# Kernel optimization log

Measured on AMD Instinct MI355X. Metric: run time of the kernel, lower is better.

Reference implementation:

```python
import jax, jax.numpy as jnp
import numpy as np

B, N, D, L, K, H = 64, 576, 768, 64, 5, 8  # batch, tokens, dim, out_token_len, knn k, heads
HD = D // H
SCALE = HD ** -0.5


def layer_norm(x, g, b, eps=1e-5):
    m = jnp.mean(x, axis=-1, keepdims=True)
    v = jnp.mean((x - m) ** 2, axis=-1, keepdims=True)
    return (x - m) * jax.lax.rsqrt(v + eps) * g + b


def cluster(feat, noise):
    # DPC-KNN: pairwise distances, k-NN density, parent distance, peak selection
    sq = jnp.sum(feat * feat, axis=-1)  # [B,N]
    dm = sq[:, :, None] + sq[:, None, :] - 2.0 * jnp.einsum('bnd,bmd->bnm', feat, feat)
    dm = jnp.sqrt(jnp.maximum(dm, 0.0)) / jnp.sqrt(jnp.asarray(D, feat.dtype))  # [B,N,N]
    neg_near, _ = jax.lax.top_k(-dm, K)                       # k smallest distances (negated)
    density = jnp.exp(-jnp.mean(neg_near ** 2, axis=-1))      # [B,N]
    density = density + noise * 1e-6                          # deterministic tie-break
    mask = (density[:, None, :] > density[:, :, None]).astype(feat.dtype)
    dist_max = jnp.max(dm.reshape(dm.shape[0], -1), axis=-1)[:, None, None]
    dist = jnp.min(dm * mask + dist_max * (1.0 - mask), axis=-1)  # [B,N]
    score = dist * density
    _, idx_down = jax.lax.top_k(score, L)                     # [B,L] cluster centers
    dm_down = jnp.take_along_axis(dm, idx_down[:, :, None], axis=1)  # [B,L,N]
    idx_cluster = jnp.argmin(dm_down, axis=1)                 # [B,N] assign to nearest center
    idx_cluster = idx_cluster.at[jnp.arange(dm.shape[0])[:, None], idx_down].set(
        jnp.arange(L)[None, :])
    return idx_cluster


def merger(feat, idx_cluster, token_score):
    b, n, d = feat.shape
    idx = (idx_cluster + jnp.arange(b)[:, None] * L).reshape(-1)       # [B*N]
    tw = jnp.exp(token_score)                                          # [B,N,1]
    all_w = jax.ops.segment_sum(tw.reshape(-1, 1), idx, num_segments=b * L) + 1e-6
    norm_w = tw / all_w[idx].reshape(b, n, 1)
    merged = jax.ops.segment_sum((feat * norm_w).reshape(-1, d), idx, num_segments=b * L)
    return merged.reshape(b, L, d)


def setup_inputs() -> dict:
    key = jax.random.key(0)
    ks = jax.random.split(key, 16)
    s = 0.02
    return {
        'x': jax.random.normal(ks[0], (B, N, D), jnp.float32),
        'density_noise': jax.random.uniform(ks[1], (B, N), jnp.float32),
        'norm1_g': jnp.ones((D,), jnp.float32),
        'norm1_b': jnp.zeros((D,), jnp.float32),
        'score_w': s * jax.random.normal(ks[2], (D, 1), jnp.float32),
        'score_b': jnp.zeros((1,), jnp.float32),
        'wq': s * jax.random.normal(ks[3], (D, D), jnp.float32),
        'wk': s * jax.random.normal(ks[4], (D, D), jnp.float32),
        'wv': s * jax.random.normal(ks[5], (D, D), jnp.float32),
        'proj_w': s * jax.random.normal(ks[6], (D, D), jnp.float32),
        'proj_b': jnp.zeros((D,), jnp.float32),
        'norm2_g': jnp.ones((D,), jnp.float32),
        'norm2_b': jnp.zeros((D,), jnp.float32),
        'fc1_w': s * jax.random.normal(ks[7], (D, 4 * D), jnp.float32),
        'fc1_b': jnp.zeros((4 * D,), jnp.float32),
        'fc2_w': s * jax.random.normal(ks[8], (4 * D, D), jnp.float32),
        'fc2_b': jnp.zeros((D,), jnp.float32),
    }


def reference(x, density_noise, norm1_g, norm1_b, score_w, score_b, wq, wk, wv,
              proj_w, proj_b, norm2_g, norm2_b, fc1_w, fc1_b, fc2_w, fc2_b):
    xn = layer_norm(x, norm1_g, norm1_b)                 # [B,N,D]
    token_score = xn @ score_w + score_b                 # [B,N,1]
    idx_cluster = cluster(jax.lax.stop_gradient(xn), density_noise)  # no-grad in torch
    q_input = merger(xn, idx_cluster, token_score)       # [B,L,D]
    kv = xn
    # STMAttention: cross-attn with token_score bias added to logits
    q = (q_input @ wq).reshape(B, L, H, HD).transpose(0, 2, 1, 3)
    k = (kv @ wk).reshape(B, N, H, HD).transpose(0, 2, 1, 3)
    v = (kv @ wv).reshape(B, N, H, HD).transpose(0, 2, 1, 3)
    dots = jnp.einsum('bhid,bhjd->bhij', q, k) * SCALE   # [B,H,L,N]
    bias = token_score[:, :, 0][:, None, None, :]        # [B,1,1,N]
    attn = jax.nn.softmax(dots + bias, axis=-1)
    out = jnp.einsum('bhij,bhjd->bhid', attn, v)
    out = out.transpose(0, 2, 1, 3).reshape(B, L, D)
    out = out @ proj_w + proj_b
    feature = q_input + out
    h = layer_norm(feature, norm2_g, norm2_b)
    h = jax.nn.gelu(h @ fc1_w + fc1_b, approximate=False) @ fc2_w + fc2_b
    return feature + h
```

## Files before the change

kernel.cpp:

```cpp
#include <hip/hip_runtime.h>
#include <math.h>

#define B_   64
#define N_   576
#define D_   768
#define L_   64
#define H_   8
#define HD_  96
#define NB_  (B_*N_)
#define ML_  (B_*L_)
#define KV_STRIDE_ 1536
#define SCALE_ 0.10206207f
#define INV_SQRT_D_ 0.03608439182f
#define LO_SCALE_ 4.8828125e-4f

typedef __attribute__((ext_vector_type(8))) _Float16 half8v;
typedef __attribute__((ext_vector_type(4))) float floatx4;

__device__ __forceinline__ unsigned short f2h(float f) {
  _Float16 h = (_Float16)f;
  unsigned short u; __builtin_memcpy(&u, &h, 2);
  return u;
}
__device__ __forceinline__ float h2f(unsigned short u) {
  _Float16 h; __builtin_memcpy(&h, &u, 2);
  return (float)h;
}
__device__ __forceinline__ void gload_lds16(const void* g, void* l) {
  __builtin_amdgcn_global_load_lds(
      (const __attribute__((address_space(1))) unsigned*)g,
      (__attribute__((address_space(3))) unsigned*)l, 16, 0, 0);
}

__global__ __launch_bounds__(256) void k_ln1(const float* __restrict__ x,
    const float* __restrict__ g, const float* __restrict__ bt,
    const float* __restrict__ sw, const float* __restrict__ sb,
    unsigned short* __restrict__ xh, unsigned short* __restrict__ xl,
    float* __restrict__ ts, float* __restrict__ sq)
{
  int row = blockIdx.x, tid = threadIdx.x;
  const float* xr = x + (size_t)row * D_;
  float v0 = xr[tid], v1 = xr[tid + 256], v2 = xr[tid + 512];
  __shared__ float r1[256], r2[256];
  r1[tid] = v0 + v1 + v2;
  r2[tid] = v0 * v0 + v1 * v1 + v2 * v2;
  __syncthreads();
  for (int o = 128; o > 0; o >>= 1) {
    if (tid < o) { r1[tid] += r1[tid + o]; r2[tid] += r2[tid + o]; }
    __syncthreads();
  }
  float mean = r1[0] * (1.0f / D_);
  float var  = r2[0] * (1.0f / D_) - mean * mean;
  float rstd = rsqrtf(var + 1e-5f);
  __syncthreads();
  float o0 = (v0 - mean) * rstd * g[tid      ] + bt[tid      ];
  float o1 = (v1 - mean) * rstd * g[tid + 256] + bt[tid + 256];
  float o2 = (v2 - mean) * rstd * g[tid + 512] + bt[tid + 512];
  auto split = [](float o, unsigned short& hu, unsigned short& lu) {
    _Float16 h = (_Float16)o;
    float hf = (float)h;
    _Float16 l = (_Float16)((o - hf) * 2048.0f);
    __builtin_memcpy(&hu, &h, 2);
    __builtin_memcpy(&lu, &l, 2);
  };
  unsigned short h0, l0, h1, l1, h2, l2;
  split(o0, h0, l0); split(o1, h1, l1); split(o2, h2, l2);
  unsigned short* xho = xh + (size_t)row * D_;
  unsigned short* xlo = xl + (size_t)row * D_;
  xho[tid] = h0; xho[tid + 256] = h1; xho[tid + 512] = h2;
  xlo[tid] = l0; xlo[tid + 256] = l1; xlo[tid + 512] = l2;
  r1[tid] = o0 * sw[tid] + o1 * sw[tid + 256] + o2 * sw[tid + 512];
  r2[tid] = o0 * o0 + o1 * o1 + o2 * o2;
  __syncthreads();
  for (int o = 128; o > 0; o >>= 1) {
    if (tid < o) { r1[tid] += r1[tid + o]; r2[tid] += r2[tid + o]; }
    __syncthreads();
  }
  if (tid == 0) { ts[row] = r1[0] + sb[0]; sq[row] = r2[0]; }
}

__global__ __launch_bounds__(256) void k_dmg(const unsigned short* __restrict__ xh,
    const unsigned short* __restrict__ xl, const float* __restrict__ sq,
    float* __restrict__ dm, float* __restrict__ dmax)
{
  __shared__ __align__(16) unsigned short S[4][96 * 64];
  int b = blockIdx.y;
  int t = blockIdx.x, ti = 0, rl = 6;
  while (t >= rl) { t -= rl; ++ti; --rl; }
  int tj = ti + t;
  int tid = threadIdx.x;
  int wave = tid >> 6, lane = tid & 63;
  int wr = (wave >> 1) * 48, wc = (wave & 1) * 48;
  int mloc = lane & 15, quad = lane >> 4;
  size_t rowA = (size_t)b * N_ + ti * 96;
  size_t rowB = (size_t)b * N_ + tj * 96;

  const unsigned short* srcbase =
      (wave == 0) ? xh + rowA * D_ :
      (wave == 1) ? xl + rowA * D_ :
      (wave == 2) ? xh + rowB * D_ : xl + rowB * D_;
  int lrow = lane >> 3, lchunk = lane & 7;
  const unsigned short* gsrc0 = srcbase + (size_t)lrow * D_ + ((lchunk ^ lrow) * 8);
  unsigned short* lbase = &S[wave][0];

  floatx4 a1[3][3], a2[3][3];
#pragma unroll
  for (int i = 0; i < 3; ++i)
#pragma unroll
    for (int j = 0; j < 3; ++j) {
      a1[i][j] = (floatx4){0.f, 0.f, 0.f, 0.f};
      a2[i][j] = (floatx4){0.f, 0.f, 0.f, 0.f};
    }

  for (int kt = 0; kt < D_; kt += 64) {
    __syncthreads();
#pragma unroll
    for (int rb = 0; rb < 12; ++rb)
      gload_lds16(gsrc0 + (size_t)rb * 8 * D_ + kt, lbase + rb * 8 * 64);
    __syncthreads();
#pragma unroll
    for (int ks = 0; ks < 2; ++ks) {
      half8v ah[3], al[3], bh[3], bl[3];
      int cperm = (((ks << 2) | quad) ^ (mloc & 7)) * 8;
#pragma unroll
      for (int i = 0; i < 3; ++i) {
        int ro = (wr + i * 16 + mloc) * 64 + cperm;
        ah[i] = *(const half8v*)&S[0][ro];
        al[i] = *(const half8v*)&S[1][ro];
      }
#pragma unroll
      for (int j = 0; j < 3; ++j) {
        int ro = (wc + j * 16 + mloc) * 64 + cperm;
        bh[j] = *(const half8v*)&S[2][ro];
        bl[j] = *(const half8v*)&S[3][ro];
      }
#pragma unroll
      for (int i = 0; i < 3; ++i)
#pragma unroll
        for (int j = 0; j < 3; ++j) {
          a1[i][j] = __builtin_amdgcn_mfma_f32_16x16x32_f16(ah[i], bh[j], a1[i][j], 0, 0, 0);
          a2[i][j] = __builtin_amdgcn_mfma_f32_16x16x32_f16(ah[i], bl[j], a2[i][j], 0, 0, 0);
          a2[i][j] = __builtin_amdgcn_mfma_f32_16x16x32_f16(al[i], bh[j], a2[i][j], 0, 0, 0);
        }
    }
  }

  const float* sqb = sq + b * N_;
  float* dmb = dm + (size_t)b * N_ * N_;
  bool diag = (ti == tj);
  float vmax = 0.f;
#pragma unroll
  for (int j = 0; j < 3; ++j) {
    int gj = tj * 96 + wc + j * 16 + mloc;
    float sj = sqb[gj];
#pragma unroll
    for (int i = 0; i < 3; ++i) {
      int gi0 = ti * 96 + wr + i * 16 + quad * 4;
#pragma unroll
      for (int reg = 0; reg < 4; ++reg) {
        int gi = gi0 + reg;
        float g = a1[i][j][reg] + a2[i][j][reg] * LO_SCALE_;
        float d = sqb[gi] + sj - 2.0f * g;
        float v = sqrtf(fmaxf(d, 0.0f)) * INV_SQRT_D_;
        vmax = fmaxf(vmax, v);
        if (!diag || gj >= gi) {
          dmb[(size_t)gi * N_ + gj] = v;
          dmb[(size_t)gj * N_ + gi] = v;
        }
      }
    }
  }
#pragma unroll
  for (int msk = 32; msk >= 1; msk >>= 1) vmax = fmaxf(vmax, __shfl_xor(vmax, msk));
  if (lane == 0) atomicMax((unsigned int*)(dmax + b), __float_as_uint(vmax));
}

__global__ __launch_bounds__(64) void k_density(const float* __restrict__ dm,
    const float* __restrict__ noise, float* __restrict__ den)
{
  int row = blockIdx.x, lane = threadIdx.x;
  const float* r = dm + (size_t)row * N_;
  float a0 = 1e30f, a1 = 1e30f, a2 = 1e30f, a3 = 1e30f, a4 = 1e30f;
  auto ins5 = [&](float xv) {
    a4 = fminf(a4, xv);
    float t;
    t = fminf(a3, a4); a4 = fmaxf(a3, a4); a3 = t;
    t = fminf(a2, a3); a3 = fmaxf(a2, a3); a2 = t;
    t = fminf(a1, a2); a2 = fmaxf(a1, a2); a1 = t;
    t = fminf(a0, a1); a1 = fmaxf(a0, a1); a0 = t;
  };
#pragma unroll
  for (int t = 0; t < 9; ++t) ins5(r[lane + 64 * t]);
  for (int m = 1; m < 64; m <<= 1) {
    float b0 = __shfl_xor(a0, m), b1 = __shfl_xor(a1, m), b2 = __shfl_xor(a2, m);
    float b3 = __shfl_xor(a3, m), b4 = __shfl_xor(a4, m);
    ins5(b0); ins5(b1); ins5(b2); ins5(b3); ins5(b4);
  }
  if (lane == 0) {
    float ms = (a0 * a0 + a1 * a1 + a2 * a2 + a3 * a3 + a4 * a4) * 0.2f;
    den[row] = expf(-ms) + noise[row] * 1e-6f;
  }
}

__global__ __launch_bounds__(64) void k_dist(const float* __restrict__ dm,
    const float* __restrict__ den, const float* __restrict__ dmax,
    float* __restrict__ score)
{
  int row = blockIdx.x, lane = threadIdx.x;
  int b = row / N_;
  float di = den[row], dx = dmax[b];
  const float* r = dm + (size_t)row * N_;
  const float* db = den + b * N_;
  float m = dx;
#pragma unroll
  for (int t = 0; t < 9; ++t) {
    int j = lane + 64 * t;
    float v = (db[j] > di) ? r[j] : dx;
    m = fminf(m, v);
  }
  for (int msk = 1; msk < 64; msk <<= 1) m = fminf(m, __shfl_xor(m, msk));
  if (lane == 0) score[row] = m * di;
}

__global__ __launch_bounds__(256) void k_topL(const float* __restrict__ score,
    int* __restrict__ idxd)
{
  int b = blockIdx.x, tid = threadIdx.x;
  __shared__ float s[N_];
  __shared__ float rv[256];
  __shared__ int   ri[256];
  for (int j = tid; j < N_; j += 256) s[j] = score[b * N_ + j];
  __syncthreads();
  for (int it = 0; it < L_; ++it) {
    float bv = -1e30f; int bi = 1 << 30;
    for (int j = tid; j < N_; j += 256) {
      float v = s[j];
      if (v > bv || (v == bv && j < bi)) { bv = v; bi = j; }
    }
    rv[tid] = bv; ri[tid] = bi; __syncthreads();
    for (int o = 128; o > 0; o >>= 1) {
      if (tid < o) {
        float v2 = rv[tid + o]; int i2 = ri[tid + o];
        if (v2 > rv[tid] || (v2 == rv[tid] && i2 < ri[tid])) { rv[tid] = v2; ri[tid] = i2; }
      }
      __syncthreads();
    }
    if (tid == 0) { idxd[b * L_ + it] = ri[0]; s[ri[0]] = -1e30f; }
    __syncthreads();
  }
}

__global__ __launch_bounds__(576) void k_assign(const float* __restrict__ dm,
    const int* __restrict__ idxd, int* __restrict__ idxc)
{
  int b = blockIdx.x, n = threadIdx.x;
  __shared__ int ctr[L_];
  if (n < L_) ctr[n] = idxd[b * L_ + n];
  __syncthreads();
  const float* dmb = dm + (size_t)b * N_ * N_;
  float best = 1e30f; int bl = 0;
  for (int l = 0; l < L_; ++l) {
    float v = dmb[(size_t)ctr[l] * N_ + n];
    if (v < best) { best = v; bl = l; }
  }
  for (int l = 0; l < L_; ++l)
    if (ctr[l] == n) bl = l;
  idxc[b * N_ + n] = bl;
}

__global__ __launch_bounds__(256) void k_merge(const unsigned short* __restrict__ xh,
    const unsigned short* __restrict__ xl,
    const float* __restrict__ ts, const int* __restrict__ idxc,
    float* __restrict__ qin)
{
  int blk = blockIdx.x;
  int b = blk >> 6, l = blk & 63;
  int tid = threadIdx.x;
  const int* ic = idxc + b * N_;
  const float* tsb = ts + b * N_;
  const unsigned short* xhb = xh + (size_t)b * N_ * D_;
  const unsigned short* xlb = xl + (size_t)b * N_ * D_;
  float a0 = 0.f, a1 = 0.f, a2 = 0.f, wsum = 0.f;
  for (int n = 0; n < N_; ++n) {
    if (ic[n] == l) {
      float w = expf(tsb[n]);
      wsum += w;
      const unsigned short* hr = xhb + (size_t)n * D_;
      const unsigned short* lr = xlb + (size_t)n * D_;
      float x0 = h2f(hr[tid      ]) + h2f(lr[tid      ]) * LO_SCALE_;
      float x1 = h2f(hr[tid + 256]) + h2f(lr[tid + 256]) * LO_SCALE_;
      float x2 = h2f(hr[tid + 512]) + h2f(lr[tid + 512]) * LO_SCALE_;
      a0 += w * x0; a1 += w * x1; a2 += w * x2;
    }
  }
  float inv = 1.0f / (wsum + 1e-6f);
  float* q = qin + (size_t)blk * D_;
  q[tid] = a0 * inv; q[tid + 256] = a1 * inv; q[tid + 512] = a2 * inv;
}

__global__ __launch_bounds__(256) void k_wt(const float* __restrict__ W,
    unsigned short* __restrict__ WT, int K, int N)
{
  __shared__ float t[32][33];
  int k0 = blockIdx.x * 32, n0 = blockIdx.y * 32;
  int tid = threadIdx.x;
  int r = tid >> 3, c4 = (tid & 7) * 4;
  float4 v = *(const float4*)(W + (size_t)(k0 + r) * N + n0 + c4);
  t[r][c4] = v.x; t[r][c4 + 1] = v.y; t[r][c4 + 2] = v.z; t[r][c4 + 3] = v.w;
  __syncthreads();
  ushort4 s4;
  s4.x = f2h(t[c4 + 0][r]); s4.y = f2h(t[c4 + 1][r]);
  s4.z = f2h(t[c4 + 2][r]); s4.w = f2h(t[c4 + 3][r]);
  *(ushort4*)(WT + (size_t)(n0 + r) * K + k0 + c4) = s4;
}

template<int EPI, int ASRC>
__global__ __launch_bounds__(256) void k_mgemm(const void* __restrict__ Ap_,
    const unsigned short* __restrict__ Wt, const float* __restrict__ bias,
    const float* __restrict__ res, void* __restrict__ outp,
    int M, int Nd, int Kd)
{
  __shared__ __align__(16) unsigned short As[128 * 64];
  __shared__ __align__(16) unsigned short Bs[128 * 64];
  int tid = threadIdx.x;
  int bm = blockIdx.x * 128, bn = blockIdx.y * 128;
  int wave = tid >> 6, lane = tid & 63;
  int wr = (wave >> 1) * 64, wc = (wave & 1) * 64;
  int mloc = lane & 15, quad = lane >> 4;

  floatx4 acc[4][4];
#pragma unroll
  for (int i = 0; i < 4; ++i)
#pragma unroll
    for (int j = 0; j < 4; ++j)
      acc[i][j] = (floatx4){0.f, 0.f, 0.f, 0.f};

  int lrow = lane >> 3, lchunk = lane & 7;
  const unsigned short* bsrc0 =
      Wt + (size_t)(bn + wave * 32 + lrow) * Kd + ((lchunk ^ lrow) * 8);
  unsigned short* bdst0 = &Bs[(wave * 32) * 64];
  const unsigned short* asrc0 = (ASRC == 1)
      ? (const unsigned short*)Ap_ + (size_t)(bm + wave * 32 + lrow) * Kd + ((lchunk ^ lrow) * 8)
      : nullptr;
  unsigned short* adst0 = &As[(wave * 32) * 64];

  for (int kt = 0; kt < Kd; kt += 64) {
    __syncthreads();
#pragma unroll
    for (int rb = 0; rb < 4; ++rb)
      gload_lds16(bsrc0 + (size_t)rb * 8 * Kd + kt, bdst0 + rb * 8 * 64);
    if (ASRC == 1) {
#pragma unroll
      for (int rb = 0; rb < 4; ++rb)
        gload_lds16(asrc0 + (size_t)rb * 8 * Kd + kt, adst0 + rb * 8 * 64);
    } else {
      const float* A = (const float*)Ap_;
#pragma unroll
      for (int it = 0; it < 4; ++it) {
        int idx = tid + it * 256;
        int r = idx >> 3, c = idx & 7;
        const float* ap = A + (size_t)(bm + r) * Kd + kt + c * 8;
        float4 f0 = *(const float4*)ap;
        float4 f1 = *(const float4*)(ap + 4);
        uint4 pk;
        pk.x = (unsigned)f2h(f0.x) | ((unsigned)f2h(f0.y) << 16);
        pk.y = (unsigned)f2h(f0.z) | ((unsigned)f2h(f0.w) << 16);
        pk.z = (unsigned)f2h(f1.x) | ((unsigned)f2h(f1.y) << 16);
        pk.w = (unsigned)f2h(f1.z) | ((unsigned)f2h(f1.w) << 16);
        *(uint4*)&As[r * 64 + ((c ^ (r & 7)) * 8)] = pk;
      }
    }
    __syncthreads();
#pragma unroll
    for (int ks = 0; ks < 2; ++ks) {
      half8v af[4], bf[4];
      int cperm = (((ks << 2) | quad) ^ (mloc & 7)) * 8;
#pragma unroll
      for (int i = 0; i < 4; ++i)
        af[i] = *(const half8v*)&As[(wr + i * 16 + mloc) * 64 + cperm];
#pragma unroll
      for (int j = 0; j < 4; ++j)
        bf[j] = *(const half8v*)&Bs[(wc + j * 16 + mloc) * 64 + cperm];
#pragma unroll
      for (int i = 0; i < 4; ++i)
#pragma unroll
        for (int j = 0; j < 4; ++j)
          acc[i][j] = __builtin_amdgcn_mfma_f32_16x16x32_f16(af[i], bf[j], acc[i][j], 0, 0, 0);
    }
  }

  float bv[4] = {0.f, 0.f, 0.f, 0.f};
  if (EPI >= 1) {
#pragma unroll
    for (int j = 0; j < 4; ++j) bv[j] = bias[bn + wc + j * 16 + mloc];
  }
#pragma unroll
  for (int i = 0; i < 4; ++i) {
    int gr0 = bm + wr + i * 16 + quad * 4;
#pragma unroll
    for (int j = 0; j < 4; ++j) {
      int gcn = bn + wc + j * 16 + mloc;
#pragma unroll
      for (int reg = 0; reg < 4; ++reg) {
        float v = acc[i][j][reg];
        size_t off = (size_t)(gr0 + reg) * Nd + gcn;
        if (EPI == 0) {
          ((unsigned short*)outp)[off] = f2h(v);
        } else if (EPI == 1) {
          ((float*)outp)[off] = v + bv[j] + res[off];
        } else {
          v += bv[j];
          v = 0.5f * v * (1.0f + erff(v * 0.70710678f));
          ((unsigned short*)outp)[off] = f2h(v);
        }
      }
    }
  }
}

__global__ __launch_bounds__(256) void k_attn(const unsigned short* __restrict__ Qu,
    const unsigned short* __restrict__ KVu, const float* __restrict__ ts,
    float* __restrict__ aout)
{
  __shared__ __align__(16) unsigned short Ks[64 * 104];
  __shared__ __align__(16) unsigned short VsT[96 * 64];
  __shared__ __align__(16) unsigned short sPa[64 * 64];
  __shared__ float tsb[64];
  int h = blockIdx.x, b = blockIdx.y;
  int tid = threadIdx.x;
  int wave = tid >> 6, lane = tid & 63;
  int mloc = lane & 15, quad = lane >> 4;

  half8v qf[3];
  {
    const unsigned short* qrow = Qu + (size_t)(b * 64 + wave * 16 + mloc) * D_ + h * 96 + quad * 8;
#pragma unroll
    for (int k = 0; k < 3; ++k) qf[k] = *(const half8v*)(qrow + k * 32);
  }

  floatx4 of[6];
#pragma unroll
  for (int dt = 0; dt < 6; ++dt) of[dt] = (floatx4){0.f, 0.f, 0.f, 0.f};
  float m[4], l[4];
#pragma unroll
  for (int r = 0; r < 4; ++r) { m[r] = -1e30f; l[r] = 0.f; }

  for (int jt = 0; jt < 9; ++jt) {
    int j0 = jt * 64;
    __syncthreads();
#pragma unroll
    for (int t = 0; t < 3; ++t) {
      int id = tid + t * 256;
      int row = id / 12, c = id % 12;
      *(uint4*)&Ks[row * 104 + c * 8] =
          *(const uint4*)(KVu + (size_t)(b * N_ + j0 + row) * KV_STRIDE_ + h * 96 + c * 8);
    }
#pragma unroll
    for (int t = 0; t < 3; ++t) {
      int id = tid + t * 256;
      int keyp = id & 31, dq = (id >> 5) * 4;
      int key = keyp * 2;
      const unsigned short* vp =
          KVu + (size_t)(b * N_ + j0 + key) * KV_STRIDE_ + 768 + h * 96 + dq;
      ushort4 v0 = *(const ushort4*)vp;
      ushort4 v1 = *(const ushort4*)(vp + KV_STRIDE_);
      unsigned pk0 = (unsigned)v0.x | ((unsigned)v1.x << 16);
      unsigned pk1 = (unsigned)v0.y | ((unsigned)v1.y << 16);
      unsigned pk2 = (unsigned)v0.z | ((unsigned)v1.z << 16);
      unsigned pk3 = (unsigned)v0.w | ((unsigned)v1.w << 16);
      int cbase = key >> 3, off = key & 7;
#pragma unroll
      for (int i = 0; i < 4; ++i) {
        int d = dq + i;
        unsigned pv = (i == 0) ? pk0 : (i == 1) ? pk1 : (i == 2) ? pk2 : pk3;
        *(unsigned*)&VsT[d * 64 + ((cbase ^ (d & 7)) << 3) + off] = pv;
      }
    }
    if (tid < 64) tsb[tid] = ts[b * N_ + j0 + tid];
    __syncthreads();

    floatx4 acc[4];
#pragma unroll
    for (int j = 0; j < 4; ++j) acc[j] = (floatx4){0.f, 0.f, 0.f, 0.f};
#pragma unroll
    for (int j = 0; j < 4; ++j)
#pragma unroll
      for (int k = 0; k < 3; ++k) {
        half8v kf = *(const half8v*)&Ks[(j * 16 + mloc) * 104 + k * 32 + quad * 8];
        acc[j] = __builtin_amdgcn_mfma_f32_16x16x32_f16(qf[k], kf, acc[j], 0, 0, 0);
      }

    float ts4[4];
#pragma unroll
    for (int j = 0; j < 4; ++j) ts4[j] = tsb[j * 16 + mloc];
    float rm[4] = {-1e30f, -1e30f, -1e30f, -1e30f};
#pragma unroll
    for (int j = 0; j < 4; ++j)
#pragma unroll
      for (int r = 0; r < 4; ++r) {
        acc[j][r] = acc[j][r] * SCALE_ + ts4[j];
        rm[r] = fmaxf(rm[r], acc[j][r]);
      }
#pragma unroll
    for (int r = 0; r < 4; ++r) {
      rm[r] = fmaxf(rm[r], __shfl_xor(rm[r], 1));
      rm[r] = fmaxf(rm[r], __shfl_xor(rm[r], 2));
      rm[r] = fmaxf(rm[r], __shfl_xor(rm[r], 4));
      rm[r] = fmaxf(rm[r], __shfl_xor(rm[r], 8));
    }
    float alpha[4], rs[4];
#pragma unroll
    for (int r = 0; r < 4; ++r) {
      float mn = fmaxf(m[r], rm[r]);
      alpha[r] = __expf(m[r] - mn);
      m[r] = mn;
      rs[r] = 0.f;
    }
#pragma unroll
    for (int j = 0; j < 4; ++j)
#pragma unroll
      for (int r = 0; r < 4; ++r) {
        float p = __expf(acc[j][r] - m[r]);
        acc[j][r] = p; rs[r] += p;
      }
#pragma unroll
    for (int r = 0; r < 4; ++r) {
      rs[r] += __shfl_xor(rs[r], 1); rs[r] += __shfl_xor(rs[r], 2);
      rs[r] += __shfl_xor(rs[r], 4); rs[r] += __shfl_xor(rs[r], 8);
      l[r] = l[r] * alpha[r] + rs[r];
    }
#pragma unroll
    for (int dt = 0; dt < 6; ++dt)
#pragma unroll
      for (int r = 0; r < 4; ++r) of[dt][r] *= alpha[r];

#pragma unroll
    for (int j = 0; j < 4; ++j)
#pragma unroll
      for (int r = 0; r < 4; ++r) {
        int row = wave * 16 + quad * 4 + r;
        int key = j * 16 + mloc;
        sPa[row * 64 + (((key >> 3) ^ (row & 7)) << 3) + (key & 7)] = f2h(acc[j][r]);
      }
    half8v pa[2];
    int prow = wave * 16 + mloc;
#pragma unroll
    for (int f2 = 0; f2 < 2; ++f2)
      pa[f2] = *(const half8v*)&sPa[prow * 64 + (((f2 * 4 + quad) ^ (prow & 7)) << 3)];
#pragma unroll
    for (int dt = 0; dt < 6; ++dt)
#pragma unroll
      for (int f2 = 0; f2 < 2; ++f2) {
        int vrow = dt * 16 + mloc;
        half8v vf = *(const half8v*)&VsT[vrow * 64 + (((f2 * 4 + quad) ^ (vrow & 7)) << 3)];
        of[dt] = __builtin_amdgcn_mfma_f32_16x16x32_f16(pa[f2], vf, of[dt], 0, 0, 0);
      }
  }

  float linv[4];
#pragma unroll
  for (int r = 0; r < 4; ++r) linv[r] = 1.0f / l[r];
#pragma unroll
  for (int dt = 0; dt < 6; ++dt)
#pragma unroll
    for (int r = 0; r < 4; ++r) {
      int row = b * 64 + wave * 16 + quad * 4 + r;
      int col = h * 96 + dt * 16 + mloc;
      aout[(size_t)row * D_ + col] = of[dt][r] * linv[r];
    }
}

__global__ __launch_bounds__(256) void k_ln2(const float* __restrict__ f,
    const float* __restrict__ g, const float* __restrict__ bt, float* __restrict__ out)
{
  int row = blockIdx.x, tid = threadIdx.x;
  const float* fr = f + (size_t)row * D_;
  float v0 = fr[tid], v1 = fr[tid + 256], v2 = fr[tid + 512];
  __shared__ float r1[256], r2[256];
  r1[tid] = v0 + v1 + v2;
  r2[tid] = v0 * v0 + v1 * v1 + v2 * v2;
  __syncthreads();
  for (int o = 128; o > 0; o >>= 1) {
    if (tid < o) { r1[tid] += r1[tid + o]; r2[tid] += r2[tid + o]; }
    __syncthreads();
  }
  float mean = r1[0] * (1.0f / D_);
  float var  = r2[0] * (1.0f / D_) - mean * mean;
  float rstd = rsqrtf(var + 1e-5f);
  float* oo = out + (size_t)row * D_;
  oo[tid      ] = (v0 - mean) * rstd * g[tid      ] + bt[tid      ];
  oo[tid + 256] = (v1 - mean) * rstd * g[tid + 256] + bt[tid + 256];
  oo[tid + 512] = (v2 - mean) * rstd * g[tid + 512] + bt[tid + 512];
}

extern "C" void kernel_launch(void* const* d_in, const int* in_sizes, int n_in,
                              void* d_out, int out_size, void* d_ws, size_t ws_size,
                              hipStream_t stream)
{
  (void)in_sizes; (void)n_in; (void)out_size; (void)ws_size;
  const float* x    = (const float*)d_in[0];
  const float* nois = (const float*)d_in[1];
  const float* n1g  = (const float*)d_in[2];
  const float* n1b  = (const float*)d_in[3];
  const float* sw   = (const float*)d_in[4];
  const float* sb   = (const float*)d_in[5];
  const float* wq   = (const float*)d_in[6];
  const float* wk   = (const float*)d_in[7];
  const float* wv   = (const float*)d_in[8];
  const float* pw   = (const float*)d_in[9];
  const float* pb   = (const float*)d_in[10];
  const float* n2g  = (const float*)d_in[11];
  const float* n2b  = (const float*)d_in[12];
  const float* f1w  = (const float*)d_in[13];
  const float* f1b  = (const float*)d_in[14];
  const float* f2w  = (const float*)d_in[15];
  const float* f2b  = (const float*)d_in[16];

  float* ws    = (float*)d_ws;
  unsigned short* XH = (unsigned short*)ws;
  unsigned short* XL = XH + (size_t)NB_ * D_;
  float* RG    = ws + (size_t)NB_ * D_;
  float* QIN   = RG + (size_t)NB_ * D_;
  float* FEAT  = QIN + (size_t)ML_ * D_;
  float* AOUT  = FEAT + (size_t)ML_ * D_;
  float* QBUF  = AOUT + (size_t)ML_ * D_;
  float* P     = QBUF + (size_t)ML_ * D_;
  unsigned short* QH16 = (unsigned short*)P;  P += (size_t)ML_ * D_ / 2;
  unsigned short* WTQ  = (unsigned short*)P;  P += (size_t)D_ * D_ / 2;
  unsigned short* WTKV = (unsigned short*)P;  P += (size_t)D_ * D_;
  unsigned short* WTP  = (unsigned short*)P;  P += (size_t)D_ * D_ / 2;
  unsigned short* WT1  = (unsigned short*)P;  P += (size_t)D_ * 4 * D_ / 2;
  unsigned short* WT2  = (unsigned short*)P;  P += (size_t)D_ * 4 * D_ / 2;
  float* TS    = P;
  float* SQ    = TS + NB_;
  float* DEN   = SQ + NB_;
  float* SCORE = DEN + NB_;
  float* DMAX  = SCORE + NB_;
  int*   IDXD  = (int*)(DMAX + 64);
  int*   IDXC  = IDXD + ML_;
  float* DM    = RG;
  unsigned short* KVB = (unsigned short*)RG;
  unsigned short* HID = (unsigned short*)RG;

  hipMemsetAsync(DMAX, 0, 64 * sizeof(float), stream);
  k_wt<<<dim3(24, 24), 256, 0, stream>>>(wq, WTQ, D_, D_);
  k_wt<<<dim3(24, 24), 256, 0, stream>>>(wk, WTKV, D_, D_);
  k_wt<<<dim3(24, 24), 256, 0, stream>>>(wv, WTKV + (size_t)D_ * D_, D_, D_);
  k_wt<<<dim3(24, 24), 256, 0, stream>>>(pw, WTP, D_, D_);
  k_wt<<<dim3(24, 96), 256, 0, stream>>>(f1w, WT1, D_, 4 * D_);
  k_wt<<<dim3(96, 24), 256, 0, stream>>>(f2w, WT2, 4 * D_, D_);

  k_ln1<<<NB_, 256, 0, stream>>>(x, n1g, n1b, sw, sb, XH, XL, TS, SQ);
  k_dmg<<<dim3(21, B_), 256, 0, stream>>>(XH, XL, SQ, DM, DMAX);
  k_density<<<NB_, 64, 0, stream>>>(DM, nois, DEN);
  k_dist<<<NB_, 64, 0, stream>>>(DM, DEN, DMAX, SCORE);
  k_topL<<<B_, 256, 0, stream>>>(SCORE, IDXD);
  k_assign<<<B_, 576, 0, stream>>>(DM, IDXD, IDXC);
  k_merge<<<ML_, 256, 0, stream>>>(XH, XL, TS, IDXC, QIN);

  k_mgemm<0, 0><<<dim3(ML_ / 128, D_ / 128), 256, 0, stream>>>(
      QIN, WTQ, nullptr, nullptr, QH16, ML_, D_, D_);
  k_mgemm<0, 1><<<dim3(NB_ / 128, KV_STRIDE_ / 128), 256, 0, stream>>>(
      XH, WTKV, nullptr, nullptr, KVB, NB_, KV_STRIDE_, D_);
  k_attn<<<dim3(H_, B_), 256, 0, stream>>>(QH16, KVB, TS, AOUT);
  k_mgemm<1, 0><<<dim3(ML_ / 128, D_ / 128), 256, 0, stream>>>(
      AOUT, WTP, pb, QIN, FEAT, ML_, D_, D_);
  k_ln2<<<ML_, 256, 0, stream>>>(FEAT, n2g, n2b, QBUF);
  k_mgemm<2, 0><<<dim3(ML_ / 128, (4 * D_) / 128), 256, 0, stream>>>(
      QBUF, WT1, f1b, nullptr, HID, ML_, 4 * D_, D_);
  k_mgemm<1, 1><<<dim3(ML_ / 128, D_ / 128), 256, 0, stream>>>(
      HID, WT2, f2b, FEAT, d_out, ML_, D_, 4 * D_);
}
```

Baseline: 946.6 us.

## Replace iterative top-L selection with bitonic sort and remap dmg blocks per XCD

New measurement: 870.4 us. -8.1%, faster.

```diff
diff --git a/kernel.cpp b/kernel.cpp
--- a/kernel.cpp
+++ b/kernel.cpp
@@ -84,8 +84,11 @@
     float* __restrict__ dm, float* __restrict__ dmax)
 {
   __shared__ __align__(16) unsigned short S[4][96 * 64];
-  int b = blockIdx.y;
-  int t = blockIdx.x, ti = 0, rl = 6;
+  int flat = blockIdx.x;
+  int xcd = flat & 7, seq = flat >> 3;
+  int b = (seq / 21) * 8 + xcd;
+  int t = seq % 21;
+  int ti = 0, rl = 6;
   while (t >= rl) { t -= rl; ++ti; --rl; }
   int tj = ti + t;
   int tid = threadIdx.x;
@@ -226,28 +229,32 @@
     int* __restrict__ idxd)
 {
   int b = blockIdx.x, tid = threadIdx.x;
-  __shared__ float s[N_];
-  __shared__ float rv[256];
-  __shared__ int   ri[256];
-  for (int j = tid; j < N_; j += 256) s[j] = score[b * N_ + j];
+  __shared__ float s[1024];
+  __shared__ int   si[1024];
+  for (int i = tid; i < 1024; i += 256) {
+    s[i] = (i < N_) ? score[b * N_ + i] : -3.0e38f;
+    si[i] = i;
+  }
   __syncthreads();
-  for (int it = 0; it < L_; ++it) {
-    float bv = -1e30f; int bi = 1 << 30;
-    for (int j = tid; j < N_; j += 256) {
-      float v = s[j];
-      if (v > bv || (v == bv && j < bi)) { bv = v; bi = j; }
-    }
-    rv[tid] = bv; ri[tid] = bi; __syncthreads();
-    for (int o = 128; o > 0; o >>= 1) {
-      if (tid < o) {
-        float v2 = rv[tid + o]; int i2 = ri[tid + o];
-        if (v2 > rv[tid] || (v2 == rv[tid] && i2 < ri[tid])) { rv[tid] = v2; ri[tid] = i2; }
+  for (int k = 2; k <= 1024; k <<= 1) {
+    for (int j = k >> 1; j > 0; j >>= 1) {
+#pragma unroll
+      for (int t = 0; t < 2; ++t) {
+        int idx512 = tid + t * 256;
+        int lo = idx512 & (j - 1);
+        int i = ((idx512 ^ lo) << 1) | lo;
+        int p = i | j;
+        float as = s[i], bs = s[p];
+        int ai = si[i], bi = si[p];
+        bool bba = (bs > as) || (bs == as && bi < ai);
+        bool up = ((i & k) == 0);
+        bool dosw = up ? bba : !bba;
+        if (dosw) { s[i] = bs; s[p] = as; si[i] = bi; si[p] = ai; }
       }
       __syncthreads();
     }
-    if (tid == 0) { idxd[b * L_ + it] = ri[0]; s[ri[0]] = -1e30f; }
-    __syncthreads();
-  }
+  }
+  if (tid < L_) idxd[b * L_ + tid] = si[tid];
 }
 
 __global__ __launch_bounds__(576) void k_assign(const float* __restrict__ dm,
@@ -651,7 +658,7 @@
   k_wt<<<dim3(96, 24), 256, 0, stream>>>(f2w, WT2, 4 * D_, D_);
 
   k_ln1<<<NB_, 256, 0, stream>>>(x, n1g, n1b, sw, sb, XH, XL, TS, SQ);
-  k_dmg<<<dim3(21, B_), 256, 0, stream>>>(XH, XL, SQ, DM, DMAX);
+  k_dmg<<<1344, 256, 0, stream>>>(XH, XL, SQ, DM, DMAX);
   k_density<<<NB_, 64, 0, stream>>>(DM, nois, DEN);
   k_dist<<<NB_, 64, 0, stream>>>(DM, DEN, DMAX, SCORE);
   k_topL<<<B_, 256, 0, stream>>>(SCORE, IDXD);
```
